# Kernel tuning notes

Measured on AMD Instinct MI355X. Metric: run time of the kernel, lower is better.

Reference implementation:

```python
import jax, jax.numpy as jnp
import numpy as np

P = 3  # spline degree in both u and v (init_kwargs degrees=[3,3])


def _knot_vector(n_cp, p):
    # clamped uniform knot vector, length n_cp+p+1 (matches calculate_knot_vectors)
    kv = np.concatenate([np.zeros(p), np.linspace(0.0, 1.0, n_cp - p + 1), np.ones(p)])
    return jnp.asarray(kv.astype(np.float32))


def _basis_and_deriv(u, spans, knots, p):
    # Cox-de Boor basis functions and 1st derivatives (NURBS Book A2.3), vectorized
    # u, spans: [S,F,E]; knots: 1D. Returns (N, dN) each [S,F,E,p+1].
    left = [None] * (p + 1)
    right = [None] * (p + 1)
    ndu = [[None] * (p + 1) for _ in range(p + 1)]
    ndu[0][0] = jnp.ones_like(u)
    for j in range(1, p + 1):
        left[j] = u - knots[spans - j + 1]
        right[j] = knots[spans + j] - u
        saved = jnp.zeros_like(u)
        for r in range(j):
            ndu[j][r] = right[r + 1] + left[j - r]  # knot differences
            tmp = ndu[r][j - 1] / ndu[j][r]
            ndu[r][j] = saved + right[r + 1] * tmp
            saved = left[j - r] * tmp
        ndu[j][j] = saved
    n = 1  # nth_derivative = 1
    ders = [[jnp.zeros_like(u) for _ in range(p + 1)] for _ in range(n + 1)]
    for j in range(p + 1):
        ders[0][j] = ndu[j][p]
    for r in range(p + 1):
        a = [[jnp.zeros_like(u) for _ in range(p + 1)] for _ in range(2)]
        a[0][0] = jnp.ones_like(u)
        s1, s2 = 0, 1
        for k in range(1, n + 1):
            d = jnp.zeros_like(u)
            rk, pk = r - k, p - k
            if r >= k:
                a[s2][0] = a[s1][0] / ndu[pk + 1][rk]
                d = a[s2][0] * ndu[rk][pk]
            j1 = 1 if rk >= -1 else -rk
            j2 = k - 1 if r - 1 <= pk else p - r
            for jj in range(j1, j2 + 1):
                a[s2][jj] = (a[s1][jj] - a[s1][jj - 1]) / ndu[pk + 1][rk + jj]
                d = d + a[s2][jj] * ndu[rk + jj][pk]
            if r <= pk:
                a[s2][k] = -a[s1][k - 1] / ndu[pk + 1][r]
                d = d + a[s2][k] * ndu[r][pk]
            ders[k][r] = d
            s1, s2 = s2, s1
    # multiply by p!/(p-k)! factor for k=1
    N0 = jnp.stack(ders[0], axis=-1)
    N1 = jnp.stack([ders[1][j] * p for j in range(p + 1)], axis=-1)
    return N0, N1


def _forward(evaluation_points, control_points):
    S, F, n_u, n_v, _ = control_points.shape
    p = P
    knots_u = _knot_vector(n_u, p)
    knots_v = _knot_vector(n_v, p)
    u = evaluation_points[..., 0]
    v = evaluation_points[..., 1]
    # uniform knot span search: floor(t * n_intervals) + degree (find_spans, uniform branch)
    spans_u = jnp.clip(jnp.floor(u * (n_u - p)).astype(jnp.int32) + p, p, n_u - 1)
    spans_v = jnp.clip(jnp.floor(v * (n_v - p)).astype(jnp.int32) + p, p, n_v - 1)
    bu0, bu1 = _basis_and_deriv(u, spans_u, knots_u, p)  # [S,F,E,p+1]
    bv0, bv1 = _basis_and_deriv(v, spans_v, knots_v, p)
    offs = jnp.arange(p + 1)
    iu = spans_u[..., None] - p + offs  # [S,F,E,p+1] control indices in u
    iv = spans_v[..., None] - p + offs
    sidx = jnp.arange(S)[:, None, None, None, None]
    fidx = jnp.arange(F)[None, :, None, None, None]
    # gather local (p+1)x(p+1) control net per eval point: [S,F,E,p+1,p+1,3]
    g = control_points[sidx, fidx, iu[..., :, None], iv[..., None, :]]
    pts = jnp.einsum('sfeijc,sfei,sfej->sfec', g, bu0, bv0)
    du = jnp.einsum('sfeijc,sfei,sfej->sfec', g, bu1, bv0)
    dv = jnp.einsum('sfeijc,sfei,sfej->sfec', g, bu0, bv1)
    nrm = jnp.cross(du, dv)
    nrm = nrm / (jnp.linalg.norm(nrm, axis=-1, keepdims=True) + 1e-12)
    ones = jnp.ones_like(pts[..., :1])
    points4 = jnp.concatenate([pts, ones], axis=-1)
    normals4 = jnp.concatenate([nrm, jnp.zeros_like(ones)], axis=-1)
    return points4, normals4


def setup_inputs() -> dict:
    key = jax.random.key(0)
    k1, k2 = jax.random.split(key)
    S, F, E = 4, 4, 65536
    N_CP = 32
    evaluation_points = jax.random.uniform(k1, (S, F, E, 2), dtype=jnp.float32)
    control_points = jax.random.normal(k2, (S, F, N_CP, N_CP, 3), dtype=jnp.float32)
    return {"evaluation_points": evaluation_points, "control_points": control_points}


def reference(evaluation_points, control_points):
    return _forward(evaluation_points, control_points)
```

## Files before the change

### kernel.cpp

```cpp
#include <hip/hip_runtime.h>

typedef __fp16 half2_t __attribute__((ext_vector_type(2)));

#define S_DIM 4
#define F_DIM 4
#define E_DIM 65536
#define NCP   32

union H2U { unsigned u; half2_t h; };

__device__ __forceinline__ unsigned pkh(float a, float b) {
    H2U c; c.h = __builtin_amdgcn_cvt_pkrtz(a, b);
    return c.u;
}
__device__ __forceinline__ half2_t ash2(unsigned u) {
    H2U c; c.u = u;
    return c.h;
}

__device__ __forceinline__ void basis3(float u, float fs, float* N0, float* N1) {
    const float h = 1.0f / 29.0f;
    const float b = fs * h;
    const float L1 = u - b;
    const float L2 = u - fmaxf(b - h, 0.0f);
    const float L3 = u - fmaxf(b - 2.0f * h, 0.0f);
    const float R1 = (b + h) - u;
    const float R2 = fminf(b + 2.0f * h, 1.0f) - u;
    const float R3 = fminf(b + 3.0f * h, 1.0f) - u;

    const float r1h = 29.0f, r2h = 14.5f, r3h = 29.0f / 3.0f;
    const bool lo0 = fs < 0.5f,  lo1 = fs < 1.5f;
    const bool hi0 = fs > 27.5f, hi1 = fs > 26.5f;
    const float i10 = r1h;
    const float i20 = lo0 ? r1h : r2h;
    const float i21 = hi0 ? r1h : r2h;
    const float i30 = lo0 ? r1h : (lo1 ? r2h : r3h);
    const float i31 = (lo0 || hi0) ? r2h : r3h;
    const float i32 = hi0 ? r1h : (hi1 ? r2h : r3h);

    const float v01 = R1 * i10;
    const float v11 = L1 * i10;
    float t = v01 * i20;
    const float v02 = R1 * t;
    float s = L2 * t;
    t = v11 * i21;
    const float v12 = s + R2 * t;
    const float v22 = L1 * t;
    t = v02 * i30;
    N0[0] = R1 * t;
    s = L3 * t;
    t = v12 * i31;
    N0[1] = s + R2 * t;
    s = L2 * t;
    t = v22 * i32;
    N0[2] = s + R3 * t;
    N0[3] = L1 * t;
    const float a0 = v02 * i30, a1 = v12 * i31, a2 = v22 * i32;
    N1[0] = -3.0f * a0;
    N1[1] = 3.0f * (a0 - a1);
    N1[2] = 3.0f * (a1 - a2);
    N1[3] = 3.0f * a2;
}

__global__ __launch_bounds__(256) void nurbs_eval_kernel(
    const float* __restrict__ ep,
    const float* __restrict__ cp,
    float* __restrict__ out)
{
    __shared__ unsigned sm[3 * 32 * 33];

    const int sf  = blockIdx.y;
    const int tid = threadIdx.x;

    const int su_ = tid >> 3, sm_ = tid & 7;
    const float* rowp = cp + ((size_t)sf * 1024 + (size_t)su_ * 32) * 3;
    const int o = 12 * sm_;
    const float4 Ld0 = *(const float4*)(rowp + o);
    const float4 Ld1 = *(const float4*)(rowp + o + 4);
    const float4 Ld2 = *(const float4*)(rowp + o + 8);
    const float4 Ld3 = *(const float4*)(rowp + ((sm_ == 7) ? 80 : (o + 12)));

    const int e   = blockIdx.x * 256 + tid;
    const int idx = sf * E_DIM + e;

    const float2 uvp = ((const float2*)ep)[idx];
    const float uu = uvp.x, vv = uvp.y;

    const float fsu = fminf(fmaxf(floorf(uu * 29.0f), 0.0f), 28.0f);
    const float fsv = fminf(fmaxf(floorf(vv * 29.0f), 0.0f), 28.0f);
    const int bu = (int)fsu, bv = (int)fsv;

    float bu0[4], bu1[4], bv0[4], bv1[4];
    basis3(uu, fsu, bu0, bu1);
    basis3(vv, fsv, bv0, bv1);

    const half2_t w00 = __builtin_amdgcn_cvt_pkrtz(bv0[0], bv0[1]);
    const half2_t w01 = __builtin_amdgcn_cvt_pkrtz(bv0[2], bv0[3]);
    const half2_t w10 = __builtin_amdgcn_cvt_pkrtz(bv1[0], bv1[1]);
    const half2_t w11 = __builtin_amdgcn_cvt_pkrtz(bv1[2], bv1[3]);

    {
        float f[16];
        f[0]=Ld0.x; f[1]=Ld0.y; f[2]=Ld0.z; f[3]=Ld0.w;
        f[4]=Ld1.x; f[5]=Ld1.y; f[6]=Ld1.z; f[7]=Ld1.w;
        f[8]=Ld2.x; f[9]=Ld2.y; f[10]=Ld2.z; f[11]=Ld2.w;
        f[12]=Ld3.x; f[13]=Ld3.y; f[14]=Ld3.z; f[15]=Ld3.w;
        unsigned* E0w = sm;
        unsigned* E1w = sm + 1056;
        unsigned* E2w = sm + 2112;
#pragma unroll
        for (int ee = 0; ee < 4; ++ee) {
            const int v = 4 * sm_ + ee;
            const int a = su_ * 33 + v;
            E0w[a] = pkh(f[3*ee+0], f[3*ee+3]);
            E1w[a] = pkh(f[3*ee+1], f[3*ee+4]);
            E2w[a] = pkh(f[3*ee+2], f[3*ee+5]);
        }
    }
    __syncthreads();

    const unsigned* E0 = sm;
    const unsigned* E1 = sm + 1056;
    const unsigned* E2 = sm + 2112;
    const int base = 33 * bu + bv;

    float px=0.f, py=0.f, pz=0.f;
    float dux=0.f, duy=0.f, duz=0.f;
    float dvx=0.f, dvy=0.f, dvz=0.f;

#pragma unroll
    for (int i = 0; i < 4; ++i) {
        const int a = base + 33 * i;
        const half2_t x0 = ash2(E0[a]), x1 = ash2(E0[a + 2]);
        const half2_t y0 = ash2(E1[a]), y1 = ash2(E1[a + 2]);
        const half2_t z0 = ash2(E2[a]), z1 = ash2(E2[a + 2]);
        const float t0x = __builtin_amdgcn_fdot2(x1, w01, __builtin_amdgcn_fdot2(x0, w00, 0.0f, false), false);
        const float t1x = __builtin_amdgcn_fdot2(x1, w11, __builtin_amdgcn_fdot2(x0, w10, 0.0f, false), false);
        const float t0y = __builtin_amdgcn_fdot2(y1, w01, __builtin_amdgcn_fdot2(y0, w00, 0.0f, false), false);
        const float t1y = __builtin_amdgcn_fdot2(y1, w11, __builtin_amdgcn_fdot2(y0, w10, 0.0f, false), false);
        const float t0z = __builtin_amdgcn_fdot2(z1, w01, __builtin_amdgcn_fdot2(z0, w00, 0.0f, false), false);
        const float t1z = __builtin_amdgcn_fdot2(z1, w11, __builtin_amdgcn_fdot2(z0, w10, 0.0f, false), false);
        px  = fmaf(bu0[i], t0x, px);  py  = fmaf(bu0[i], t0y, py);  pz  = fmaf(bu0[i], t0z, pz);
        dux = fmaf(bu1[i], t0x, dux); duy = fmaf(bu1[i], t0y, duy); duz = fmaf(bu1[i], t0z, duz);
        dvx = fmaf(bu0[i], t1x, dvx); dvy = fmaf(bu0[i], t1y, dvy); dvz = fmaf(bu0[i], t1z, dvz);
    }

    float nx = duy * dvz - duz * dvy;
    float ny = duz * dvx - dux * dvz;
    float nz = dux * dvy - duy * dvx;
    float n2 = nx * nx + ny * ny + nz * nz;
    const float du2 = dux*dux + duy*duy + duz*duz;
    const float dv2 = dvx*dvx + dvy*dvy + dvz*dvz;

    if (n2 < 2e-2f * (du2 * dv2)) {
        const float* patch = cp + (size_t)sf * 3072;
        float DUX=0.f, DUY=0.f, DUZ=0.f, DVX=0.f, DVY=0.f, DVZ=0.f;
#pragma unroll
        for (int i = 0; i < 4; ++i) {
            float s0x=0.f, s0y=0.f, s0z=0.f, s1x=0.f, s1y=0.f, s1z=0.f;
#pragma unroll
            for (int j = 0; j < 4; ++j) {
                const float* p = patch + (((bu + i) * 32) + (bv + j)) * 3;
                const float gx = p[0], gy = p[1], gz = p[2];
                s0x = fmaf(gx, bv0[j], s0x); s0y = fmaf(gy, bv0[j], s0y); s0z = fmaf(gz, bv0[j], s0z);
                s1x = fmaf(gx, bv1[j], s1x); s1y = fmaf(gy, bv1[j], s1y); s1z = fmaf(gz, bv1[j], s1z);
            }
            DUX = fmaf(bu1[i], s0x, DUX); DUY = fmaf(bu1[i], s0y, DUY); DUZ = fmaf(bu1[i], s0z, DUZ);
            DVX = fmaf(bu0[i], s1x, DVX); DVY = fmaf(bu0[i], s1y, DVY); DVZ = fmaf(bu0[i], s1z, DVZ);
        }
        nx = DUY * DVZ - DUZ * DVY;
        ny = DUZ * DVX - DUX * DVZ;
        nz = DUX * DVY - DUY * DVX;
        n2 = nx * nx + ny * ny + nz * nz;
    }

    const float inv = __builtin_amdgcn_rsqf(fmaxf(n2, 1e-24f));
    nx *= inv; ny *= inv; nz *= inv;

    float4* outv = (float4*)out;
    outv[idx] = make_float4(px, py, pz, 1.0f);
    outv[(size_t)S_DIM * F_DIM * E_DIM + idx] = make_float4(nx, ny, nz, 0.0f);
}

extern "C" void kernel_launch(void* const* d_in, const int* in_sizes, int n_in,
                              void* d_out, int out_size, void* d_ws, size_t ws_size,
                              hipStream_t stream) {
    const float* ep = (const float*)d_in[0];
    const float* cp = (const float*)d_in[1];
    float* out = (float*)d_out;

    dim3 grid(E_DIM / 256, S_DIM * F_DIM);
    dim3 block(256);
    hipLaunchKernelGGL(nurbs_eval_kernel, grid, block, 0, stream, ep, cp, out);
}
```

Before: 20.65 us.

## Use nontemporal stores, rcp-based basis, RTN fp16 packing, lower fallback threshold

Output writes become nontemporal stores so the streaming results do not pollute the cache. The eval-point load is issued before the control-point loads. The basis denominators are now computed with hardware reciprocals instead of table selects, and fp16 packing switches from round-toward-zero to round-to-nearest conversion, which should reduce error. The fallback threshold for the fp32 normal recompute is lowered from 2e-2 to 4e-3, so fewer threads take the slow path, at the risk of less accurate normals.

```diff
diff --git a/kernel.cpp b/kernel.cpp
--- a/kernel.cpp
+++ b/kernel.cpp
@@ -1,6 +1,7 @@
 #include <hip/hip_runtime.h>
 
 typedef __fp16 half2_t __attribute__((ext_vector_type(2)));
+typedef float f32x4 __attribute__((ext_vector_type(4)));
 
 #define S_DIM 4
 #define F_DIM 4
@@ -10,12 +11,16 @@
 union H2U { unsigned u; half2_t h; };
 
 __device__ __forceinline__ unsigned pkh(float a, float b) {
-    H2U c; c.h = __builtin_amdgcn_cvt_pkrtz(a, b);
+    H2U c; c.h.x = (__fp16)a; c.h.y = (__fp16)b;
     return c.u;
 }
 __device__ __forceinline__ half2_t ash2(unsigned u) {
     H2U c; c.u = u;
     return c.h;
+}
+__device__ __forceinline__ half2_t mkw(float a, float b) {
+    half2_t h; h.x = (__fp16)a; h.y = (__fp16)b;
+    return h;
 }
 
 __device__ __forceinline__ void basis3(float u, float fs, float* N0, float* N1) {
@@ -27,31 +32,26 @@
     const float R1 = (b + h) - u;
     const float R2 = fminf(b + 2.0f * h, 1.0f) - u;
     const float R3 = fminf(b + 3.0f * h, 1.0f) - u;
-
-    const float r1h = 29.0f, r2h = 14.5f, r3h = 29.0f / 3.0f;
-    const bool lo0 = fs < 0.5f,  lo1 = fs < 1.5f;
-    const bool hi0 = fs > 27.5f, hi1 = fs > 26.5f;
-    const float i10 = r1h;
-    const float i20 = lo0 ? r1h : r2h;
-    const float i21 = hi0 ? r1h : r2h;
-    const float i30 = lo0 ? r1h : (lo1 ? r2h : r3h);
-    const float i31 = (lo0 || hi0) ? r2h : r3h;
-    const float i32 = hi0 ? r1h : (hi1 ? r2h : r3h);
-
+    const float i10 = __builtin_amdgcn_rcpf(R1 + L1);
     const float v01 = R1 * i10;
     const float v11 = L1 * i10;
+    const float i20 = __builtin_amdgcn_rcpf(R1 + L2);
     float t = v01 * i20;
     const float v02 = R1 * t;
     float s = L2 * t;
+    const float i21 = __builtin_amdgcn_rcpf(R2 + L1);
     t = v11 * i21;
     const float v12 = s + R2 * t;
     const float v22 = L1 * t;
+    const float i30 = __builtin_amdgcn_rcpf(R1 + L3);
     t = v02 * i30;
     N0[0] = R1 * t;
     s = L3 * t;
+    const float i31 = __builtin_amdgcn_rcpf(R2 + L2);
     t = v12 * i31;
     N0[1] = s + R2 * t;
     s = L2 * t;
+    const float i32 = __builtin_amdgcn_rcpf(R3 + L1);
     t = v22 * i32;
     N0[2] = s + R3 * t;
     N0[3] = L1 * t;
@@ -72,6 +72,10 @@
     const int sf  = blockIdx.y;
     const int tid = threadIdx.x;
 
+    const int e   = blockIdx.x * 256 + tid;
+    const int idx = sf * E_DIM + e;
+    const float2 uvp = ((const float2*)ep)[idx];
+
     const int su_ = tid >> 3, sm_ = tid & 7;
     const float* rowp = cp + ((size_t)sf * 1024 + (size_t)su_ * 32) * 3;
     const int o = 12 * sm_;
@@ -80,10 +84,6 @@
     const float4 Ld2 = *(const float4*)(rowp + o + 8);
     const float4 Ld3 = *(const float4*)(rowp + ((sm_ == 7) ? 80 : (o + 12)));
 
-    const int e   = blockIdx.x * 256 + tid;
-    const int idx = sf * E_DIM + e;
-
-    const float2 uvp = ((const float2*)ep)[idx];
     const float uu = uvp.x, vv = uvp.y;
 
     const float fsu = fminf(fmaxf(floorf(uu * 29.0f), 0.0f), 28.0f);
@@ -94,10 +94,10 @@
     basis3(uu, fsu, bu0, bu1);
     basis3(vv, fsv, bv0, bv1);
 
-    const half2_t w00 = __builtin_amdgcn_cvt_pkrtz(bv0[0], bv0[1]);
-    const half2_t w01 = __builtin_amdgcn_cvt_pkrtz(bv0[2], bv0[3]);
-    const half2_t w10 = __builtin_amdgcn_cvt_pkrtz(bv1[0], bv1[1]);
-    const half2_t w11 = __builtin_amdgcn_cvt_pkrtz(bv1[2], bv1[3]);
+    const half2_t w00 = mkw(bv0[0], bv0[1]);
+    const half2_t w01 = mkw(bv0[2], bv0[3]);
+    const half2_t w10 = mkw(bv1[0], bv1[1]);
+    const half2_t w11 = mkw(bv1[2], bv1[3]);
 
     {
         float f[16];
@@ -152,7 +152,7 @@
     const float du2 = dux*dux + duy*duy + duz*duz;
     const float dv2 = dvx*dvx + dvy*dvy + dvz*dvz;
 
-    if (n2 < 2e-2f * (du2 * dv2)) {
+    if (n2 < 4e-3f * (du2 * dv2)) {
         const float* patch = cp + (size_t)sf * 3072;
         float DUX=0.f, DUY=0.f, DUZ=0.f, DVX=0.f, DVY=0.f, DVZ=0.f;
 #pragma unroll
@@ -177,9 +177,11 @@
     const float inv = __builtin_amdgcn_rsqf(fmaxf(n2, 1e-24f));
     nx *= inv; ny *= inv; nz *= inv;
 
-    float4* outv = (float4*)out;
-    outv[idx] = make_float4(px, py, pz, 1.0f);
-    outv[(size_t)S_DIM * F_DIM * E_DIM + idx] = make_float4(nx, ny, nz, 0.0f);
+    f32x4* outv = (f32x4*)out;
+    f32x4 pt; pt[0]=px; pt[1]=py; pt[2]=pz; pt[3]=1.0f;
+    f32x4 nm; nm[0]=nx; nm[1]=ny; nm[2]=nz; nm[3]=0.0f;
+    __builtin_nontemporal_store(pt, &outv[idx]);
+    __builtin_nontemporal_store(nm, &outv[(size_t)S_DIM * F_DIM * E_DIM + idx]);
 }
 
 extern "C" void kernel_launch(void* const* d_in, const int* in_sizes, int n_in,
```

After: 18.19 us (median of 2 runs). 1.14x faster.
